# Kernel tuning notes

Hardware: AMD Instinct MI355X
Metric: run time of the kernel (lower is better)

## Reference

```python
import jax, jax.numpy as jnp
import numpy as np

N_USER = 50000
N_ITEM = 50000
E = 400000
IN = 128
OUT = 128
H = 2
C = OUT // H
SLOPE = 0.2
LN_EPS = 1e-5


def setup_inputs() -> dict:
    key = jax.random.key(0)
    ks = jax.random.split(key, 20)
    s = 0.05
    d = {
        'x_user': jax.random.normal(ks[0], (N_USER, IN), jnp.float32),
        'x_item': jax.random.normal(ks[1], (N_ITEM, IN), jnp.float32),
        'ei_u2i': jnp.stack([jax.random.randint(ks[2], (E,), 0, N_USER),
                             jax.random.randint(ks[3], (E,), 0, N_ITEM)]).astype(jnp.int64),
        'ei_i2u': jnp.stack([jax.random.randint(ks[4], (E,), 0, N_ITEM),
                             jax.random.randint(ks[5], (E,), 0, N_USER)]).astype(jnp.int64),
        # GATConv params for edge type user->item
        'w_src_u2i': jax.random.normal(ks[6], (IN, OUT), jnp.float32) * s,
        'w_dst_u2i': jax.random.normal(ks[7], (IN, OUT), jnp.float32) * s,
        'att_src_u2i': jax.random.normal(ks[8], (H, C), jnp.float32) * s,
        'att_dst_u2i': jax.random.normal(ks[9], (H, C), jnp.float32) * s,
        'b_u2i': jnp.zeros((OUT,), jnp.float32),
        # GATConv params for edge type item->user
        'w_src_i2u': jax.random.normal(ks[10], (IN, OUT), jnp.float32) * s,
        'w_dst_i2u': jax.random.normal(ks[11], (IN, OUT), jnp.float32) * s,
        'att_src_i2u': jax.random.normal(ks[12], (H, C), jnp.float32) * s,
        'att_dst_i2u': jax.random.normal(ks[13], (H, C), jnp.float32) * s,
        'b_i2u': jnp.zeros((OUT,), jnp.float32),
        # LayerNorm params per destination node type
        'ln_g_user': jnp.ones((OUT,), jnp.float32),
        'ln_b_user': jnp.zeros((OUT,), jnp.float32),
        'ln_g_item': jnp.ones((OUT,), jnp.float32),
        'ln_b_item': jnp.zeros((OUT,), jnp.float32),
    }
    return d


def gat_conv(x_src, x_dst, ei, w_src, w_dst, att_s, att_d, bias, n_dst):
    # PyG GATConv (bipartite, add_self_loops=False, concat=True), eval mode (no attn dropout)
    hs = (x_src @ w_src).reshape(-1, H, C)  # [N_src, H, C]
    hd = (x_dst @ w_dst).reshape(-1, H, C)  # [N_dst, H, C]
    a_s = jnp.einsum('nhc,hc->nh', hs, att_s)  # [N_src, H]
    a_d = jnp.einsum('nhc,hc->nh', hd, att_d)  # [N_dst, H]
    src, dst = ei[0], ei[1]
    e = jax.nn.leaky_relu(a_s[src] + a_d[dst], SLOPE)  # [E, H]
    m = jax.ops.segment_max(e, dst, num_segments=n_dst)  # per-dst max for stable softmax
    e = jnp.exp(e - m[dst])
    z = jax.ops.segment_sum(e, dst, num_segments=n_dst)
    alpha = e / (z[dst] + 1e-16)  # [E, H]
    msg = hs[src] * alpha[:, :, None]  # [E, H, C]
    out = jax.ops.segment_sum(msg, dst, num_segments=n_dst)  # [N_dst, H, C]
    return out.reshape(n_dst, H * C) + bias


def layernorm_elu(h, g, b):
    mu = h.mean(-1, keepdims=True)
    var = ((h - mu) ** 2).mean(-1, keepdims=True)
    h = (h - mu) * jax.lax.rsqrt(var + LN_EPS) * g + b
    return jax.nn.elu(h)  # dropout is identity in eval mode


def reference(x_user, x_item, ei_u2i, ei_i2u,
              w_src_u2i, w_dst_u2i, att_src_u2i, att_dst_u2i, b_u2i,
              w_src_i2u, w_dst_i2u, att_src_i2u, att_dst_i2u, b_i2u,
              ln_g_user, ln_b_user, ln_g_item, ln_b_item):
    # HeteroConv(aggr='sum'): each dst type receives from exactly one edge type here
    out_item = gat_conv(x_user, x_item, ei_u2i, w_src_u2i, w_dst_u2i,
                        att_src_u2i, att_dst_u2i, b_u2i, N_ITEM)
    out_user = gat_conv(x_item, x_user, ei_i2u, w_src_i2u, w_dst_i2u,
                        att_src_i2u, att_dst_i2u, b_i2u, N_USER)
    out_user = layernorm_elu(out_user, ln_g_user, ln_b_user)
    out_item = layernorm_elu(out_item, ln_g_item, ln_b_item)
    return (out_user, out_item)
```

## Files before the change

kernel.cpp:

```cpp
#include <hip/hip_runtime.h>
#include <hip/hip_bf16.h>
#include <hip/hip_fp16.h>

#define N_NODES 50000
#define NE      400000
#define NB      196
#define GB      782
#define CPAD    16
#define ZB4     1563
#define TOTB    4692

typedef __attribute__((ext_vector_type(8))) short bf16x8;
typedef __attribute__((ext_vector_type(4))) float f32x4;

static __device__ __forceinline__ unsigned short f2bf(float f) {
    unsigned u = __float_as_uint(f);
    unsigned r = (u + 0x7fffu + ((u >> 16) & 1u)) >> 16;
    return (unsigned short)r;
}

struct P {
    const float *x_user, *x_item;
    const int   *ei_u2i, *ei_i2u;
    const float *w_src_u2i, *w_dst_u2i, *att_src_u2i, *att_dst_u2i, *b_u2i;
    const float *w_src_i2u, *w_dst_i2u, *att_src_i2u, *att_dst_i2u, *b_i2u;
    const float *ln_g_user, *ln_b_user, *ln_g_item, *ln_b_item;
    unsigned short *hs0b, *hs1b;
    unsigned short *wt0, *wt1;
    float *as0, *ad0, *as1, *ad1;
    float *v_s0, *v_d0, *v_s1, *v_d1;
    int   *cntp;
    int   *cntc0, *cntc1;
    int   *off0, *off1;
    int   *bsum;
    unsigned short *rank0, *rank1;
    unsigned short *s0, *s1;
    float *out_user, *out_item;
};

__global__ void prep_small(P p) {
    int b = blockIdx.x, tid = threadIdx.x;
    if (b < 4) {
        const float* w   = b==0? p.w_src_u2i : b==1? p.w_dst_u2i : b==2? p.w_src_i2u : p.w_dst_i2u;
        const float* att = b==0? p.att_src_u2i : b==1? p.att_dst_u2i : b==2? p.att_src_i2u : p.att_dst_i2u;
        float* v         = b==0? p.v_s0 : b==1? p.v_d0 : b==2? p.v_s1 : p.v_d1;
        int k = tid >> 1, h = tid & 1;
        float s = 0.f;
        for (int c = 0; c < 64; ++c) s += w[k*128 + h*64 + c] * att[h*64 + c];
        v[k*2 + h] = s;
    } else if (b < 6) {
        const float* w    = (b == 4) ? p.w_src_u2i : p.w_src_i2u;
        unsigned short* wt = (b == 4) ? p.wt0 : p.wt1;
        for (int s = tid; s < 2048; s += 256) {
            int c = s >> 4, g = s & 15;
            int kg = g ^ (c & 7);
            unsigned short u[8];
#pragma unroll
            for (int j = 0; j < 8; ++j) u[j] = f2bf(w[(size_t)(kg*8 + j)*128 + c]);
            uint4 pk;
            pk.x = (unsigned)u[0] | ((unsigned)u[1] << 16);
            pk.y = (unsigned)u[2] | ((unsigned)u[3] << 16);
            pk.z = (unsigned)u[4] | ((unsigned)u[5] << 16);
            pk.w = (unsigned)u[6] | ((unsigned)u[7] << 16);
            *(uint4*)(wt + (size_t)c*128 + g*8) = pk;
        }
    } else {
        int idx = (b - 6) * 256 + tid;
        if (idx < 2*N_NODES*CPAD/4)
            ((uint4*)p.cntp)[idx] = make_uint4(0,0,0,0);
    }
}

__global__ __launch_bounds__(256) void gemm_count(P p) {
    __shared__ char wlds[32768];
    int tid = threadIdx.x;
    int r3 = blockIdx.x % 3;
    int q3 = blockIdx.x / 3;

    if (r3 != 2) {
        int e = (q3*2 + r3) * 256 + tid;
        if (e < NE) {
            int d = p.ei_u2i[NE + e];
            int r = atomicAdd(&p.cntp[d*CPAD], 1);
            p.rank0[e] = (unsigned short)r;
        } else if (e < 2*NE) {
            int ee = e - NE;
            int d = p.ei_i2u[NE + ee];
            int r = atomicAdd(&p.cntp[(N_NODES + d)*CPAD], 1);
            p.rank1[ee] = (unsigned short)r;
        }
        return;
    }

    int bb  = q3;
    int t   = bb >= GB;
    int blk = bb - (t ? GB : 0);
    const float* x            = t ? p.x_item : p.x_user;
    const unsigned short* wt  = t ? p.wt1 : p.wt0;
    unsigned short* hs        = t ? p.hs1b : p.hs0b;
    const float2* vsa = (const float2*)(t ? p.v_s1 : p.v_s0);
    const float2* vda = (const float2*)(t ? p.v_d0 : p.v_d1);
    float2* as_out = (float2*)(t ? p.as1 : p.as0);
    float2* ad_out = (float2*)(t ? p.ad0 : p.ad1);

#pragma unroll
    for (int it = 0; it < 8; ++it) {
        int off = (tid + it*256) * 16;
        *(uint4*)(wlds + off) = *(const uint4*)((const char*)wt + off);
    }

    int lane = tid & 63, wave = tid >> 6;
    int q = lane >> 4, m = lane & 15;
    int r0 = blk*64 + wave*16;
    int row = r0 + m;
    int rowc = row < N_NODES ? row : N_NODES - 1;
    const float4* xr = (const float4*)(x + (size_t)rowc*128);

    float4 xa[8];
#pragma unroll
    for (int kk = 0; kk < 4; ++kk) {
        xa[kk*2]   = xr[kk*8 + q*2];
        xa[kk*2+1] = xr[kk*8 + q*2 + 1];
    }
    const float* xf = (const float*)xa;

    float as0 = 0.f, as1 = 0.f, ad0 = 0.f, ad1 = 0.f;
#pragma unroll
    for (int kk = 0; kk < 4; ++kk)
#pragma unroll
        for (int jj = 0; jj < 8; ++jj) {
            int k = kk*32 + q*8 + jj;
            float xv = xf[kk*8 + jj];
            float2 vs = vsa[k], vd = vda[k];
            as0 += xv*vs.x; as1 += xv*vs.y;
            ad0 += xv*vd.x; ad1 += xv*vd.y;
        }
#pragma unroll
    for (int o = 16; o < 64; o <<= 1) {
        as0 += __shfl_xor(as0, o); as1 += __shfl_xor(as1, o);
        ad0 += __shfl_xor(ad0, o); ad1 += __shfl_xor(ad1, o);
    }
    if (q == 0 && row < N_NODES) {
        as_out[row] = make_float2(as0, as1);
        ad_out[row] = make_float2(ad0, ad1);
    }

    bf16x8 af[4];
#pragma unroll
    for (int kk = 0; kk < 4; ++kk)
#pragma unroll
        for (int jj = 0; jj < 8; ++jj)
            af[kk][jj] = (short)f2bf(xf[kk*8 + jj]);

    __syncthreads();

    f32x4 acc[8];
#pragma unroll
    for (int cb = 0; cb < 8; ++cb) acc[cb] = (f32x4){0.f, 0.f, 0.f, 0.f};

#pragma unroll
    for (int cb = 0; cb < 8; ++cb) {
        int c = cb*16 + m;
#pragma unroll
        for (int kk = 0; kk < 4; ++kk) {
            int gs = (kk*4 + q) ^ (c & 7);
            bf16x8 bf = *(const bf16x8*)(wlds + (size_t)c*256 + gs*16);
            acc[cb] = __builtin_amdgcn_mfma_f32_16x16x32_bf16(af[kk], bf, acc[cb], 0, 0, 0);
        }
    }

#pragma unroll
    for (int cb = 0; cb < 8; ++cb)
#pragma unroll
        for (int reg = 0; reg < 4; ++reg) {
            int rr = r0 + q*4 + reg;
            if (rr < N_NODES) {
                __half hv = __float2half(acc[cb][reg]);
                hs[(size_t)rr*128 + cb*16 + m] = __half_as_ushort(hv);
            }
        }
}

__global__ void scan_a(P p) {
    int t = blockIdx.x / NB, j = blockIdx.x % NB;
    const int* cp = p.cntp + (t ? (size_t)N_NODES*CPAD : 0);
    int i = j*256 + threadIdx.x;
    int v = (i < N_NODES) ? cp[(size_t)i*CPAD] : 0;
    __shared__ int sd[256];
    sd[threadIdx.x] = v; __syncthreads();
    for (int off = 128; off; off >>= 1) {
        if (threadIdx.x < off) sd[threadIdx.x] += sd[threadIdx.x + off];
        __syncthreads();
    }
    if (threadIdx.x == 0) p.bsum[t*256 + j] = sd[0];
}

__global__ void scan_c(P p) {
    int t = blockIdx.x / NB, j = blockIdx.x % NB, tid = threadIdx.x;
    const int* cp = p.cntp + (t ? (size_t)N_NODES*CPAD : 0);
    int* off = t ? p.off1 : p.off0;
    int* cc  = t ? p.cntc1 : p.cntc0;

    __shared__ int sb[256];
    int bv = (tid < NB) ? p.bsum[t*256 + tid] : 0;
    sb[tid] = bv; __syncthreads();
    for (int o = 1; o < 256; o <<= 1) {
        int u = (tid >= o) ? sb[tid - o] : 0;
        __syncthreads();
        sb[tid] += u;
        __syncthreads();
    }
    int base = (j > 0) ? sb[j-1] : 0;

    int i = j*256 + tid;
    int v = (i < N_NODES) ? cp[(size_t)i*CPAD] : 0;
    __shared__ int sd[256];
    sd[tid] = v; __syncthreads();
    for (int o = 1; o < 256; o <<= 1) {
        int u = (tid >= o) ? sd[tid - o] : 0;
        __syncthreads();
        sd[tid] += u;
        __syncthreads();
    }
    if (i < N_NODES) { off[i] = base + sd[tid] - v; cc[i] = v; }
}

__global__ void fill_edges(P p) {
    int e = blockIdx.x * 256 + threadIdx.x;
    int t, ee;
    if (e < NE)        { t = 0; ee = e; }
    else if (e < 2*NE) { t = 1; ee = e - NE; }
    else return;
    const int* ei = t ? p.ei_i2u : p.ei_u2i;
    const int* off = t ? p.off1 : p.off0;
    const unsigned short* rank = t ? p.rank1 : p.rank0;
    unsigned short* srcs = t ? p.s1 : p.s0;
    int s = ei[ee], d = ei[NE + ee];
    int pos = off[d] + (int)rank[ee];
    srcs[pos] = (unsigned short)s;
}

__global__ __launch_bounds__(256) void aggregate(P p) {
    int lane = threadIdx.x & 63;
    int wave = threadIdx.x >> 6;
    int g = lane >> 4;
    int m = lane & 15;
    int gid = blockIdx.x*16 + wave*4 + g;
    int t = gid >= N_NODES;
    int d = gid - (t ? N_NODES : 0);
    int headhi = m >> 3;
    unsigned mo = (unsigned)m * 16;

    const char* hs = (const char*)(t ? p.hs1b : p.hs0b);
    const unsigned short* srcs = t ? p.s1 : p.s0;
    const float2* as2 = (const float2*)(t ? p.as1 : p.as0);
    const float2* ad2 = (const float2*)(t ? p.ad1 : p.ad0);
    int o = (t ? p.off1 : p.off0)[d];
    int n = (t ? p.cntc1 : p.cntc0)[d];

    float2 adv = ad2[d];
    float adh = headhi ? adv.y : adv.x;

    float acc[8];
#pragma unroll
    for (int j = 0; j < 8; ++j) acc[j] = 0.f;
    float z = 0.f;

    const unsigned short* sp = srcs + o;

#define ACC8(qq, ww) { \
        __half2 p0 = *(const __half2*)&(qq).x; \
        __half2 p1 = *(const __half2*)&(qq).y; \
        __half2 p2 = *(const __half2*)&(qq).z; \
        __half2 p3 = *(const __half2*)&(qq).w; \
        acc[0] += (ww) * __half2float(__low2half(p0)); \
        acc[1] += (ww) * __half2float(__high2half(p0)); \
        acc[2] += (ww) * __half2float(__low2half(p1)); \
        acc[3] += (ww) * __half2float(__high2half(p1)); \
        acc[4] += (ww) * __half2float(__low2half(p2)); \
        acc[5] += (ww) * __half2float(__high2half(p2)); \
        acc[6] += (ww) * __half2float(__low2half(p3)); \
        acc[7] += (ww) * __half2float(__high2half(p3)); }
#define WCOMP(aa) __expf(fmaxf(((headhi ? (aa).y : (aa).x) + adh), 0.2f*((headhi ? (aa).y : (aa).x) + adh)))

    int i = 0;
    for (; i + 8 <= n; i += 8) {
        unsigned sA = sp[i],   sB = sp[i+1], sC = sp[i+2], sD = sp[i+3];
        unsigned sE = sp[i+4], sF = sp[i+5], sG = sp[i+6], sH = sp[i+7];
        float2 aA = as2[sA], aB = as2[sB], aC = as2[sC], aD = as2[sD];
        float2 aE = as2[sE], aF = as2[sF], aG = as2[sG], aH = as2[sH];
        uint4 qA = *(const uint4*)(hs + ((sA << 8) + mo));
        uint4 qB = *(const uint4*)(hs + ((sB << 8) + mo));
        uint4 qC = *(const uint4*)(hs + ((sC << 8) + mo));
        uint4 qD = *(const uint4*)(hs + ((sD << 8) + mo));
        uint4 qE = *(const uint4*)(hs + ((sE << 8) + mo));
        uint4 qF = *(const uint4*)(hs + ((sF << 8) + mo));
        uint4 qG = *(const uint4*)(hs + ((sG << 8) + mo));
        uint4 qH = *(const uint4*)(hs + ((sH << 8) + mo));
        float wA = WCOMP(aA), wB = WCOMP(aB), wC = WCOMP(aC), wD = WCOMP(aD);
        float wE = WCOMP(aE), wF = WCOMP(aF), wG = WCOMP(aG), wH = WCOMP(aH);
        ACC8(qA, wA); ACC8(qB, wB); ACC8(qC, wC); ACC8(qD, wD);
        ACC8(qE, wE); ACC8(qF, wF); ACC8(qG, wG); ACC8(qH, wH);
        z += ((wA + wB) + (wC + wD)) + ((wE + wF) + (wG + wH));
    }
    for (; i + 4 <= n; i += 4) {
        unsigned sA = sp[i], sB = sp[i+1], sC = sp[i+2], sD = sp[i+3];
        float2 aA = as2[sA], aB = as2[sB], aC = as2[sC], aD = as2[sD];
        uint4 qA = *(const uint4*)(hs + ((sA << 8) + mo));
        uint4 qB = *(const uint4*)(hs + ((sB << 8) + mo));
        uint4 qC = *(const uint4*)(hs + ((sC << 8) + mo));
        uint4 qD = *(const uint4*)(hs + ((sD << 8) + mo));
        float wA = WCOMP(aA), wB = WCOMP(aB), wC = WCOMP(aC), wD = WCOMP(aD);
        ACC8(qA, wA); ACC8(qB, wB); ACC8(qC, wC); ACC8(qD, wD);
        z += (wA + wB) + (wC + wD);
    }
    for (; i < n; ++i) {
        unsigned sA = sp[i];
        float2 aA = as2[sA];
        uint4 qA = *(const uint4*)(hs + ((sA << 8) + mo));
        float wA = WCOMP(aA);
        ACC8(qA, wA);
        z += wA;
    }
#undef ACC8
#undef WCOMP

    float inv = 1.f / (z + 1e-16f);
    const float* bias = t ? p.b_i2u : p.b_u2i;
    const float* lg   = t ? p.ln_g_user : p.ln_g_item;
    const float* lb   = t ? p.ln_b_user : p.ln_b_item;
    float4 bv0 = *(const float4*)(bias + m*8);
    float4 bv1 = *(const float4*)(bias + m*8 + 4);
    float bvv[8] = {bv0.x,bv0.y,bv0.z,bv0.w,bv1.x,bv1.y,bv1.z,bv1.w};
    float h[8];
#pragma unroll
    for (int j = 0; j < 8; ++j) h[j] = acc[j]*inv + bvv[j];

    float s8 = 0.f;
#pragma unroll
    for (int j = 0; j < 8; ++j) s8 += h[j];
#pragma unroll
    for (int off = 1; off < 16; off <<= 1) s8 += __shfl_xor(s8, off);
    float mu = s8 * (1.f/128.f);
    float vs = 0.f;
#pragma unroll
    for (int j = 0; j < 8; ++j) { h[j] -= mu; vs += h[j]*h[j]; }
#pragma unroll
    for (int off = 1; off < 16; off <<= 1) vs += __shfl_xor(vs, off);
    float rstd = rsqrtf(vs * (1.f/128.f) + 1e-5f);

    float4 gv0 = *(const float4*)(lg + m*8);
    float4 gv1 = *(const float4*)(lg + m*8 + 4);
    float4 lb0 = *(const float4*)(lb + m*8);
    float4 lb1 = *(const float4*)(lb + m*8 + 4);
    float gvv[8] = {gv0.x,gv0.y,gv0.z,gv0.w,gv1.x,gv1.y,gv1.z,gv1.w};
    float lbb[8] = {lb0.x,lb0.y,lb0.z,lb0.w,lb1.x,lb1.y,lb1.z,lb1.w};
    float y[8];
#pragma unroll
    for (int j = 0; j < 8; ++j) {
        float v = h[j]*rstd*gvv[j] + lbb[j];
        y[j] = v > 0.f ? v : expm1f(v);
    }
    float* out = (t ? p.out_user : p.out_item) + (size_t)d*128 + m*8;
    *(float4*)out       = make_float4(y[0],y[1],y[2],y[3]);
    *(float4*)(out + 4) = make_float4(y[4],y[5],y[6],y[7]);
}

static inline char* carve(char*& cur, size_t bytes) {
    char* r = cur;
    cur += (bytes + 255) & ~(size_t)255;
    return r;
}

extern "C" void kernel_launch(void* const* d_in, const int* in_sizes, int n_in,
                              void* d_out, int out_size, void* d_ws, size_t ws_size,
                              hipStream_t stream) {
    P p;
    p.x_user      = (const float*)d_in[0];
    p.x_item      = (const float*)d_in[1];
    p.ei_u2i      = (const int*)d_in[2];
    p.ei_i2u      = (const int*)d_in[3];
    p.w_src_u2i   = (const float*)d_in[4];
    p.w_dst_u2i   = (const float*)d_in[5];
    p.att_src_u2i = (const float*)d_in[6];
    p.att_dst_u2i = (const float*)d_in[7];
    p.b_u2i       = (const float*)d_in[8];
    p.w_src_i2u   = (const float*)d_in[9];
    p.w_dst_i2u   = (const float*)d_in[10];
    p.att_src_i2u = (const float*)d_in[11];
    p.att_dst_i2u = (const float*)d_in[12];
    p.b_i2u       = (const float*)d_in[13];
    p.ln_g_user   = (const float*)d_in[14];
    p.ln_b_user   = (const float*)d_in[15];
    p.ln_g_item   = (const float*)d_in[16];
    p.ln_b_item   = (const float*)d_in[17];

    p.out_user = (float*)d_out;
    p.out_item = (float*)d_out + (size_t)N_NODES * 128;

    char* cur = (char*)d_ws;
    p.hs0b = (unsigned short*)carve(cur, (size_t)N_NODES*128*2);
    p.hs1b = (unsigned short*)carve(cur, (size_t)N_NODES*128*2);
    p.wt0  = (unsigned short*)carve(cur, 128*128*2);
    p.wt1  = (unsigned short*)carve(cur, 128*128*2);
    p.as0  = (float*)carve(cur, (size_t)N_NODES*2*4);
    p.ad0  = (float*)carve(cur, (size_t)N_NODES*2*4);
    p.as1  = (float*)carve(cur, (size_t)N_NODES*2*4);
    p.ad1  = (float*)carve(cur, (size_t)N_NODES*2*4);
    p.v_s0 = (float*)carve(cur, 256*4);
    p.v_d0 = (float*)carve(cur, 256*4);
    p.v_s1 = (float*)carve(cur, 256*4);
    p.v_d1 = (float*)carve(cur, 256*4);
    p.cntp = (int*)carve(cur, (size_t)2*N_NODES*CPAD*4);
    p.cntc0 = (int*)carve(cur, (size_t)N_NODES*4);
    p.cntc1 = (int*)carve(cur, (size_t)N_NODES*4);
    p.off0 = (int*)carve(cur, (size_t)N_NODES*4);
    p.off1 = (int*)carve(cur, (size_t)N_NODES*4);
    p.bsum = (int*)carve(cur, 2*256*4);
    p.rank0 = (unsigned short*)carve(cur, (size_t)NE*2);
    p.rank1 = (unsigned short*)carve(cur, (size_t)NE*2);
    p.s0   = (unsigned short*)carve(cur, (size_t)NE*2);
    p.s1   = (unsigned short*)carve(cur, (size_t)NE*2);

    prep_small<<<6 + ZB4, 256, 0, stream>>>(p);
    gemm_count<<<TOTB, 256, 0, stream>>>(p);
    scan_a<<<2*NB, 256, 0, stream>>>(p);
    scan_c<<<2*NB, 256, 0, stream>>>(p);
    fill_edges<<<(2*NE + 255)/256, 256, 0, stream>>>(p);
    aggregate<<<(2*N_NODES)/16, 256, 0, stream>>>(p);
}
```

Measured before the change: 116.0 us.

## Replace global atomic degree counting with per-block LDS histograms and byte-packed prefix

Destination-degree counting moves from padded global atomics, which also required zeroing a large padded counter array, into 128 blocks that each build a shared-memory histogram over a 6250-edge chunk using 16-bit packed LDS atomics. The per-chunk counts are stored as bytes and prefix-summed across chunks inside the GEMM launch. That yields total counts plus per-chunk offsets, which fill_edges adds to the local rank. This removes global atomic contention and the zeroing pass, at the cost of an extra 12.8 MB of byte histogram traffic and one more gather in fill_edges. It assumes per-chunk counts and per-node prefix sums fit in 8 bits.

```diff
diff --git a/kernel.cpp b/kernel.cpp
--- a/kernel.cpp
+++ b/kernel.cpp
@@ -6,9 +6,10 @@
 #define NE      400000
 #define NB      196
 #define GB      782
-#define CPAD    16
-#define ZB4     1563
-#define TOTB    4692
+#define GHIST   64
+#define EPB     6250
+#define HB      128
+#define SCB     98
 
 typedef __attribute__((ext_vector_type(8))) short bf16x8;
 typedef __attribute__((ext_vector_type(4))) float f32x4;
@@ -29,7 +30,8 @@
     unsigned short *wt0, *wt1;
     float *as0, *ad0, *as1, *ad1;
     float *v_s0, *v_d0, *v_s1, *v_d1;
-    int   *cntp;
+    unsigned char *cntg;
+    unsigned char *cumc;
     int   *cntc0, *cntc1;
     int   *off0, *off1;
     int   *bsum;
@@ -38,61 +40,115 @@
     float *out_user, *out_item;
 };
 
-__global__ void prep_small(P p) {
+__global__ __launch_bounds__(512) void prep_hist(P p) {
+    __shared__ unsigned lh[N_NODES/2];
     int b = blockIdx.x, tid = threadIdx.x;
-    if (b < 4) {
-        const float* w   = b==0? p.w_src_u2i : b==1? p.w_dst_u2i : b==2? p.w_src_i2u : p.w_dst_i2u;
-        const float* att = b==0? p.att_src_u2i : b==1? p.att_dst_u2i : b==2? p.att_src_i2u : p.att_dst_i2u;
-        float* v         = b==0? p.v_s0 : b==1? p.v_d0 : b==2? p.v_s1 : p.v_d1;
-        int k = tid >> 1, h = tid & 1;
-        float s = 0.f;
-        for (int c = 0; c < 64; ++c) s += w[k*128 + h*64 + c] * att[h*64 + c];
-        v[k*2 + h] = s;
-    } else if (b < 6) {
-        const float* w    = (b == 4) ? p.w_src_u2i : p.w_src_i2u;
-        unsigned short* wt = (b == 4) ? p.wt0 : p.wt1;
-        for (int s = tid; s < 2048; s += 256) {
-            int c = s >> 4, g = s & 15;
-            int kg = g ^ (c & 7);
-            unsigned short u[8];
-#pragma unroll
-            for (int j = 0; j < 8; ++j) u[j] = f2bf(w[(size_t)(kg*8 + j)*128 + c]);
-            uint4 pk;
-            pk.x = (unsigned)u[0] | ((unsigned)u[1] << 16);
-            pk.y = (unsigned)u[2] | ((unsigned)u[3] << 16);
-            pk.z = (unsigned)u[4] | ((unsigned)u[5] << 16);
-            pk.w = (unsigned)u[6] | ((unsigned)u[7] << 16);
-            *(uint4*)(wt + (size_t)c*128 + g*8) = pk;
+
+    if (b >= HB) {
+        int bb = b - HB;
+        if (bb < 4) {
+            if (tid < 256) {
+                const float* w   = bb==0? p.w_src_u2i : bb==1? p.w_dst_u2i : bb==2? p.w_src_i2u : p.w_dst_i2u;
+                const float* att = bb==0? p.att_src_u2i : bb==1? p.att_dst_u2i : bb==2? p.att_src_i2u : p.att_dst_i2u;
+                float* v         = bb==0? p.v_s0 : bb==1? p.v_d0 : bb==2? p.v_s1 : p.v_d1;
+                int k = tid >> 1, h = tid & 1;
+                float s = 0.f;
+                for (int c = 0; c < 64; ++c) s += w[k*128 + h*64 + c] * att[h*64 + c];
+                v[k*2 + h] = s;
+            }
+        } else {
+            const float* w    = (bb == 4) ? p.w_src_u2i : p.w_src_i2u;
+            unsigned short* wt = (bb == 4) ? p.wt0 : p.wt1;
+            for (int s = tid; s < 2048; s += 512) {
+                int c = s >> 4, g = s & 15;
+                int kg = g ^ (c & 7);
+                unsigned short u[8];
+#pragma unroll
+                for (int j = 0; j < 8; ++j) u[j] = f2bf(w[(size_t)(kg*8 + j)*128 + c]);
+                uint4 pk;
+                pk.x = (unsigned)u[0] | ((unsigned)u[1] << 16);
+                pk.y = (unsigned)u[2] | ((unsigned)u[3] << 16);
+                pk.z = (unsigned)u[4] | ((unsigned)u[5] << 16);
+                pk.w = (unsigned)u[6] | ((unsigned)u[7] << 16);
+                *(uint4*)(wt + (size_t)c*128 + g*8) = pk;
+            }
         }
-    } else {
-        int idx = (b - 6) * 256 + tid;
-        if (idx < 2*N_NODES*CPAD/4)
-            ((uint4*)p.cntp)[idx] = make_uint4(0,0,0,0);
-    }
-}
-
-__global__ __launch_bounds__(256) void gemm_count(P p) {
+        return;
+    }
+
+    int t = b >= GHIST;
+    int g = b - (t ? GHIST : 0);
+    for (int i = tid; i < N_NODES/2; i += 512) lh[i] = 0;
+    __syncthreads();
+
+    const int* dsts = (t ? p.ei_i2u : p.ei_u2i) + NE;
+    unsigned short* rank = t ? p.rank1 : p.rank0;
+    int base = g * EPB;
+
+    for (int j0 = 0; j0 < 12; j0 += 8) {
+        int cnt = 12 - j0; if (cnt > 8) cnt = 8;
+        int d8[8];
+#pragma unroll
+        for (int k = 0; k < 8; ++k)
+            if (k < cnt) d8[k] = dsts[base + tid + 512*(j0+k)];
+        unsigned r8[8];
+#pragma unroll
+        for (int k = 0; k < 8; ++k)
+            if (k < cnt) {
+                unsigned sh = (unsigned)(d8[k] & 1) * 16;
+                unsigned old = atomicAdd(&lh[d8[k] >> 1], 1u << sh);
+                r8[k] = (old >> sh) & 0xffffu;
+            }
+#pragma unroll
+        for (int k = 0; k < 8; ++k)
+            if (k < cnt) rank[base + tid + 512*(j0+k)] = (unsigned short)r8[k];
+    }
+    if (tid < EPB - 12*512) {
+        int e = base + 12*512 + tid;
+        int d = dsts[e];
+        unsigned sh = (unsigned)(d & 1) * 16;
+        unsigned old = atomicAdd(&lh[d >> 1], 1u << sh);
+        rank[e] = (unsigned short)((old >> sh) & 0xffffu);
+    }
+    __syncthreads();
+
+    unsigned char* cg = p.cntg + ((size_t)t*GHIST + g) * N_NODES;
+    for (int i4 = tid; i4 < N_NODES/4; i4 += 512) {
+        unsigned a = lh[2*i4], c = lh[2*i4+1];
+        unsigned pk = (a & 0xffu) | (((a >> 16) & 0xffu) << 8)
+                    | ((c & 0xffu) << 16) | (((c >> 16) & 0xffu) << 24);
+        ((unsigned*)cg)[i4] = pk;
+    }
+}
+
+__global__ __launch_bounds__(256) void gemm_scan2a(P p) {
     __shared__ char wlds[32768];
     int tid = threadIdx.x;
-    int r3 = blockIdx.x % 3;
-    int q3 = blockIdx.x / 3;
-
-    if (r3 != 2) {
-        int e = (q3*2 + r3) * 256 + tid;
-        if (e < NE) {
-            int d = p.ei_u2i[NE + e];
-            int r = atomicAdd(&p.cntp[d*CPAD], 1);
-            p.rank0[e] = (unsigned short)r;
-        } else if (e < 2*NE) {
-            int ee = e - NE;
-            int d = p.ei_i2u[NE + ee];
-            int r = atomicAdd(&p.cntp[(N_NODES + d)*CPAD], 1);
-            p.rank1[ee] = (unsigned short)r;
+
+    if (blockIdx.x < SCB) {
+        int t = blockIdx.x >= 49;
+        int blk = blockIdx.x - (t ? 49 : 0);
+        int g4 = blk*256 + tid;
+        if (g4 < N_NODES/4) {
+            const unsigned char* cgb = p.cntg + (size_t)t*GHIST*N_NODES;
+            unsigned char* cub = p.cumc + (size_t)t*GHIST*N_NODES;
+            int t0=0, t1=0, t2=0, t3=0;
+#pragma unroll 4
+            for (int g = 0; g < GHIST; ++g) {
+                unsigned c = ((const unsigned*)(cgb + (size_t)g*N_NODES))[g4];
+                unsigned pk = (unsigned)t0 | ((unsigned)t1 << 8)
+                            | ((unsigned)t2 << 16) | ((unsigned)t3 << 24);
+                ((unsigned*)(cub + (size_t)g*N_NODES))[g4] = pk;
+                t0 += c & 0xff; t1 += (c >> 8) & 0xff;
+                t2 += (c >> 16) & 0xff; t3 += (c >> 24) & 0xff;
+            }
+            int* cc = t ? p.cntc1 : p.cntc0;
+            ((int4*)cc)[g4] = make_int4(t0, t1, t2, t3);
         }
         return;
     }
 
-    int bb  = q3;
+    int bb  = blockIdx.x - SCB;
     int t   = bb >= GB;
     int blk = bb - (t ? GB : 0);
     const float* x            = t ? p.x_item : p.x_user;
@@ -183,9 +239,9 @@
 
 __global__ void scan_a(P p) {
     int t = blockIdx.x / NB, j = blockIdx.x % NB;
-    const int* cp = p.cntp + (t ? (size_t)N_NODES*CPAD : 0);
+    const int* cnt = t ? p.cntc1 : p.cntc0;
     int i = j*256 + threadIdx.x;
-    int v = (i < N_NODES) ? cp[(size_t)i*CPAD] : 0;
+    int v = (i < N_NODES) ? cnt[i] : 0;
     __shared__ int sd[256];
     sd[threadIdx.x] = v; __syncthreads();
     for (int off = 128; off; off >>= 1) {
@@ -197,9 +253,8 @@
 
 __global__ void scan_c(P p) {
     int t = blockIdx.x / NB, j = blockIdx.x % NB, tid = threadIdx.x;
-    const int* cp = p.cntp + (t ? (size_t)N_NODES*CPAD : 0);
+    const int* cnt = t ? p.cntc1 : p.cntc0;
     int* off = t ? p.off1 : p.off0;
-    int* cc  = t ? p.cntc1 : p.cntc0;
 
     __shared__ int sb[256];
     int bv = (tid < NB) ? p.bsum[t*256 + tid] : 0;
@@ -213,7 +268,7 @@
     int base = (j > 0) ? sb[j-1] : 0;
 
     int i = j*256 + tid;
-    int v = (i < N_NODES) ? cp[(size_t)i*CPAD] : 0;
+    int v = (i < N_NODES) ? cnt[i] : 0;
     __shared__ int sd[256];
     sd[tid] = v; __syncthreads();
     for (int o = 1; o < 256; o <<= 1) {
@@ -222,7 +277,7 @@
         sd[tid] += u;
         __syncthreads();
     }
-    if (i < N_NODES) { off[i] = base + sd[tid] - v; cc[i] = v; }
+    if (i < N_NODES) off[i] = base + sd[tid] - v;
 }
 
 __global__ void fill_edges(P p) {
@@ -236,7 +291,8 @@
     const unsigned short* rank = t ? p.rank1 : p.rank0;
     unsigned short* srcs = t ? p.s1 : p.s0;
     int s = ei[ee], d = ei[NE + ee];
-    int pos = off[d] + (int)rank[ee];
+    int gb = ee / EPB;
+    int pos = off[d] + (int)p.cumc[((size_t)t*GHIST + gb)*N_NODES + d] + (int)rank[ee];
     srcs[pos] = (unsigned short)s;
 }
 
@@ -411,7 +467,8 @@
     p.v_d0 = (float*)carve(cur, 256*4);
     p.v_s1 = (float*)carve(cur, 256*4);
     p.v_d1 = (float*)carve(cur, 256*4);
-    p.cntp = (int*)carve(cur, (size_t)2*N_NODES*CPAD*4);
+    p.cntg = (unsigned char*)carve(cur, (size_t)2*GHIST*N_NODES);
+    p.cumc = (unsigned char*)carve(cur, (size_t)2*GHIST*N_NODES);
     p.cntc0 = (int*)carve(cur, (size_t)N_NODES*4);
     p.cntc1 = (int*)carve(cur, (size_t)N_NODES*4);
     p.off0 = (int*)carve(cur, (size_t)N_NODES*4);
@@ -422,8 +479,8 @@
     p.s0   = (unsigned short*)carve(cur, (size_t)NE*2);
     p.s1   = (unsigned short*)carve(cur, (size_t)NE*2);
 
-    prep_small<<<6 + ZB4, 256, 0, stream>>>(p);
-    gemm_count<<<TOTB, 256, 0, stream>>>(p);
+    prep_hist<<<HB + 6, 512, 0, stream>>>(p);
+    gemm_scan2a<<<SCB + 2*GB, 256, 0, stream>>>(p);
     scan_a<<<2*NB, 256, 0, stream>>>(p);
     scan_c<<<2*NB, 256, 0, stream>>>(p);
     fill_edges<<<(2*NE + 255)/256, 256, 0, stream>>>(p);
```

Result: faster. 102.0 us (-12.1%).
